# Optimization experiments

Hardware: AMD Instinct MI355X
Metric: run time of the kernel (lower is better)

Reference implementation:

```python
import jax, jax.numpy as jnp
import numpy as np

N = 30000        # nodes
E_EDGES = 960000 # edges (avg degree 32)
G = 16           # graphs in batch
D_IN, D_H, D_OUT = 6, 256, 256
L = 3            # GraphConv layers per expert
N_EXP, TOP_K = 8, 2


def _lin(key, fan_in, shape):
    return jax.random.normal(key, shape, dtype=jnp.float32) / np.sqrt(fan_in)


def setup_inputs() -> dict:
    key = jax.random.key(0)
    ks = jax.random.split(key, 12)
    x = jax.random.normal(ks[0], (N, D_IN), dtype=jnp.float32)
    edge_index = jax.random.randint(ks[1], (2, E_EDGES), 0, N, dtype=jnp.int64)
    batch = jnp.sort(jax.random.randint(ks[2], (N,), 0, G, dtype=jnp.int64))
    return {
        "x": x,
        "edge_index": edge_index,
        "batch": batch,
        # SharedBusEncoder: Linear(in, hidden) + ReLU
        "enc_W": _lin(ks[3], D_IN, (D_IN, D_H)),
        "enc_b": jnp.zeros((D_H,), jnp.float32),
        # BaseRouter: Linear(hidden+2, hidden) -> ReLU -> Linear(hidden, n_experts)
        "r_W1": _lin(ks[4], D_H + 2, (D_H + 2, D_H)),
        "r_b1": jnp.zeros((D_H,), jnp.float32),
        "r_W2": _lin(ks[5], D_H, (D_H, N_EXP)),
        "r_b2": jnp.zeros((N_EXP,), jnp.float32),
        # GraphConvExpert: L layers of PyG GraphConv (lin_rel on aggregated
        # neighbors + lin_root on self), stacked over [layer, expert].
        "Wrel": _lin(ks[6], D_H, (L, N_EXP, D_H, D_OUT)),
        "brel": jnp.zeros((L, N_EXP, D_OUT), jnp.float32),
        "Wroot": _lin(ks[7], D_H, (L, N_EXP, D_H, D_OUT)),
    }


def _forward(x, edge_index, batch, enc_W, enc_b, r_W1, r_b1, r_W2, r_b2,
             Wrel, brel, Wroot):
    src, dst = edge_index[0], edge_index[1]
    # encoder
    h = jax.nn.relu(x @ enc_W + enc_b)  # [N, D_H]

    # graph size features: per-node [log(#nodes), log(#edges)] of its graph
    n_g = jax.ops.segment_sum(jnp.ones((N,), jnp.float32), batch, num_segments=G)
    e_g = jax.ops.segment_sum(jnp.ones((E_EDGES,), jnp.float32), batch[src], num_segments=G)
    size = jnp.log(jnp.maximum(jnp.stack([n_g, e_g], axis=-1), 1.0))  # [G, 2]
    size_feat = size[batch]  # [N, 2]

    # router + sparse top-k routing
    r_h = jax.nn.relu(jnp.concatenate([h, size_feat], axis=-1) @ r_W1 + r_b1)
    logits = r_h @ r_W2 + r_b2            # [N, E]
    probs = jax.nn.softmax(logits, axis=-1)
    vals, idx = jax.lax.top_k(probs, TOP_K)
    vals = vals / jnp.sum(vals, axis=-1, keepdims=True)
    sparse = jnp.zeros((N, N_EXP), probs.dtype).at[
        jnp.arange(N)[:, None], idx].set(vals)  # [N, E]

    # all-expert GraphConv stacks (dense over experts, as in the original)
    agg0 = jax.ops.segment_sum(h[src], dst, num_segments=N)  # [N, D_H]
    H = jnp.einsum('nd,edf->enf', agg0, Wrel[0]) + brel[0][:, None, :] \
        + jnp.einsum('nd,edf->enf', h, Wroot[0])             # [E, N, D]
    for l in range(1, L):
        H = jax.nn.relu(H)
        A = jax.vmap(lambda hh: jax.ops.segment_sum(hh[src], dst, num_segments=N))(H)
        H = jnp.einsum('end,edf->enf', A, Wrel[l]) + brel[l][:, None, :] \
            + jnp.einsum('end,edf->enf', H, Wroot[l])

    # mask-and-sum combine
    return jnp.einsum('enf,ne->nf', H, sparse)  # [N, D_OUT]


def reference(x, edge_index, batch, enc_W, enc_b, r_W1, r_b1, r_W2, r_b2,
              Wrel, brel, Wroot):
    return _forward(x, edge_index, batch, enc_W, enc_b, r_W1, r_b1, r_W2,
                    r_b2, Wrel, brel, Wroot)
```

## Files before the change

kernel.cpp:

```cpp
#include <hip/hip_runtime.h>
#include <hip/hip_bf16.h>
#include <math.h>

#define NEXP 8
#define GNUM 16
#define DH 256

typedef __attribute__((ext_vector_type(8))) short s16x8;
typedef __attribute__((ext_vector_type(4))) float f32x4;
typedef unsigned short u16;
typedef unsigned int u32;

__device__ __forceinline__ float bitsToF(u32 b){ union{u32 u; float f;} c; c.u=b; return c.f; }
__device__ __forceinline__ u16 f2bf(float f){
  union{float f; u32 u;} c; c.f=f;
  u32 r = c.u + 0x7fffu + ((c.u>>16)&1u);
  return (u16)(r>>16);
}

#define GLOAD_LDS16(gp, lp) __builtin_amdgcn_global_load_lds( \
    (const __attribute__((address_space(1))) unsigned int*)(gp), \
    (__attribute__((address_space(3))) unsigned int*)(lp), 16, 0, 0)

__global__ void count_edges_k(const int* __restrict__ ei, const int* __restrict__ batch,
                              int* __restrict__ deg, int* __restrict__ eg, int E){
  __shared__ int leg[GNUM];
  int t = threadIdx.x;
  if (t < GNUM) leg[t] = 0;
  __syncthreads();
  int i = blockIdx.x*blockDim.x + t;
  if (i < E){
    int s = ei[i];
    int d = ei[E + i];
    atomicAdd(&deg[d], 1);
    atomicAdd(&leg[batch[s]], 1);
  }
  __syncthreads();
  if (t < GNUM){ int v = leg[t]; if (v) atomicAdd(&eg[t], v); }
}

__global__ void count_nodes_k(const int* __restrict__ batch, int* __restrict__ ng, int N){
  __shared__ int lng[GNUM];
  int t = threadIdx.x;
  if (t < GNUM) lng[t] = 0;
  __syncthreads();
  int i = blockIdx.x*blockDim.x + t;
  if (i < N) atomicAdd(&lng[batch[i]], 1);
  __syncthreads();
  if (t < GNUM){ int v = lng[t]; if (v) atomicAdd(&ng[t], v); }
}

#define SCAN_T 1024
#define SCAN_CH 32
__global__ __launch_bounds__(1024) void scan_deg_k(const int* __restrict__ deg,
    int* __restrict__ row_ptr, int* __restrict__ cursor, int N){
  __shared__ int part[SCAN_T];
  int t = threadIdx.x;
  int base = t*SCAN_CH;
  int loc[SCAN_CH];
  int s = 0;
  #pragma unroll
  for (int j=0;j<SCAN_CH;j++){
    int i = base+j;
    int v = (i<N)? deg[i] : 0;
    loc[j] = s; s += v;
  }
  part[t] = s;
  __syncthreads();
  for (int off=1; off<SCAN_T; off<<=1){
    int add = (t>=off)? part[t-off] : 0;
    __syncthreads();
    part[t] += add;
    __syncthreads();
  }
  int ex = (t==0)? 0 : part[t-1];
  #pragma unroll
  for (int j=0;j<SCAN_CH;j++){
    int i = base+j;
    if (i<N){ int v = ex + loc[j]; row_ptr[i]=v; cursor[i]=v; }
  }
  if (t == SCAN_T-1) row_ptr[N] = part[SCAN_T-1];
}

__global__ void scatter_edges_k(const int* __restrict__ ei, int* __restrict__ cursor,
                                int* __restrict__ csr_src, int E){
  int i = blockIdx.x*blockDim.x + threadIdx.x;
  if (i>=E) return;
  int s = ei[i];
  int d = ei[E + i];
  int pos = atomicAdd(&cursor[d], 1);
  csr_src[pos] = s;
}

__global__ void size_feats_k(const int* __restrict__ ng, const int* __restrict__ eg,
                             float* __restrict__ sizef){
  int g = threadIdx.x;
  if (g < GNUM){
    sizef[g*2]   = logf(fmaxf((float)ng[g], 1.f));
    sizef[g*2+1] = logf(fmaxf((float)eg[g], 1.f));
  }
}

__global__ void mark_fail_k(float* out){ out[0] = __builtin_nanf(""); }

__global__ __launch_bounds__(256) void encoder_k(const float* __restrict__ x,
    const float* __restrict__ W, const float* __restrict__ b,
    float* __restrict__ hf, u16* __restrict__ bh, int N){
  int n = blockIdx.x; if (n>=N) return;
  int f = threadIdx.x;
  float acc = b[f];
  #pragma unroll
  for (int k=0;k<6;k++) acc += x[n*6+k]*W[k*DH+f];
  acc = fmaxf(acc, 0.f);
  hf[(size_t)n*DH+f] = acc;
  bh[(size_t)n*DH+f] = f2bf(acc);
}

__global__ __launch_bounds__(256) void convw_k(const float* __restrict__ Wrel,
    const float* __restrict__ Wroot, u16* __restrict__ WT){
  __shared__ float tile[64][65];
  int tx = threadIdx.x;
  int ty = threadIdx.y;
  int kt = blockIdx.x & 3, ct = blockIdx.x >> 2;
  int srcRoot = blockIdx.y;
  int le = blockIdx.z;
  const float* src = (srcRoot ? Wroot : Wrel) + (size_t)le*65536;
  #pragma unroll
  for (int i=0;i<16;i++){
    int kl = ty + i*4;
    tile[kl][tx] = src[(size_t)(kt*64 + kl)*256 + ct*64 + tx];
  }
  __syncthreads();
  u16* dst = WT + (size_t)le*131072 + (srcRoot ? 256 : 0) + kt*64;
  #pragma unroll
  for (int i=0;i<16;i++){
    int cl = ty + i*4;
    dst[(size_t)(ct*64 + cl)*512 + tx] = f2bf(tile[tx][cl]);
  }
}

#define R1N 32
__global__ __launch_bounds__(256) void router1_k(
    const float* __restrict__ hf, const float* __restrict__ sizef,
    const int* __restrict__ batch,
    const float* __restrict__ W1, const float* __restrict__ b1,
    float* __restrict__ rh, int N)
{
  __shared__ float xin[R1N][264];
  int t = threadIdx.x;
  int lane = t & 63, w = t >> 6;
  int n0 = blockIdx.x * R1N;
  #pragma unroll
  for (int i=0;i<R1N;i++){
    int n = n0 + i;
    xin[i][t] = (n<N) ? hf[(size_t)n*DH + t] : 0.f;
  }
  if (t < R1N){
    int n = n0 + t;
    int g = (n<N) ? (int)batch[n] : 0;
    xin[t][256] = sizef[g*2];
    xin[t][257] = sizef[g*2+1];
    xin[t][258] = 0.f; xin[t][259] = 0.f;
    xin[t][260] = 0.f; xin[t][261] = 0.f; xin[t][262] = 0.f; xin[t][263] = 0.f;
  }
  __syncthreads();

  int wn = w*8;
  float bb[4];
  #pragma unroll
  for (int c=0;c<4;c++) bb[c] = b1[lane + c*64];
  float acc[8][4];
  #pragma unroll
  for (int i=0;i<8;i++)
    #pragma unroll
    for (int c=0;c<4;c++) acc[i][c] = bb[c];

  #pragma unroll 2
  for (int k4=0; k4<256; k4+=4){
    float w4[4][4];
    #pragma unroll
    for (int j=0;j<4;j++)
      #pragma unroll
      for (int c=0;c<4;c++)
        w4[j][c] = W1[(size_t)(k4+j)*DH + lane + c*64];
    #pragma unroll
    for (int i=0;i<8;i++){
      f32x4 xv = *(const f32x4*)&xin[wn+i][k4];
      #pragma unroll
      for (int j=0;j<4;j++)
        #pragma unroll
        for (int c=0;c<4;c++)
          acc[i][c] += xv[j]*w4[j][c];
    }
  }
  float w256[4], w257[4];
  #pragma unroll
  for (int c=0;c<4;c++){
    w256[c] = W1[(size_t)256*DH + lane + c*64];
    w257[c] = W1[(size_t)257*DH + lane + c*64];
  }
  #pragma unroll
  for (int i=0;i<8;i++){
    float s0 = xin[wn+i][256], s1 = xin[wn+i][257];
    #pragma unroll
    for (int c=0;c<4;c++) acc[i][c] += s0*w256[c] + s1*w257[c];
  }
  #pragma unroll
  for (int i=0;i<8;i++){
    int n = n0 + wn + i;
    if (n < N){
      #pragma unroll
      for (int c=0;c<4;c++)
        rh[(size_t)n*DH + lane + c*64] = fmaxf(acc[i][c], 0.f);
    }
  }
}

__global__ __launch_bounds__(256) void router2_k(
    const float* __restrict__ rh, const float* __restrict__ W2,
    const float* __restrict__ b2,
    int* __restrict__ ridx, float* __restrict__ rval, int N)
{
  __shared__ float w2s[NEXP][260];
  int t = threadIdx.x;
  for (int i=t; i<NEXP*DH; i+=256){
    int e = i >> 8, k = i & 255;
    w2s[e][k] = W2[(size_t)k*NEXP + e];
  }
  __syncthreads();
  int lane = t & 63, w = t >> 6;
  int n = blockIdx.x*4 + w;
  if (n >= N) return;
  const float* r = rh + (size_t)n*DH;
  float p[NEXP];
  #pragma unroll
  for (int e=0;e<NEXP;e++) p[e] = 0.f;
  #pragma unroll
  for (int c=0;c<4;c++){
    int k = lane + c*64;
    float rv = r[k];
    #pragma unroll
    for (int e=0;e<NEXP;e++) p[e] += rv * w2s[e][k];
  }
  #pragma unroll
  for (int off=1; off<64; off<<=1){
    #pragma unroll
    for (int e=0;e<NEXP;e++) p[e] += __shfl_xor(p[e], off, 64);
  }
  if (lane == 0){
    float l0[NEXP];
    #pragma unroll
    for (int e=0;e<NEXP;e++) l0[e] = p[e] + b2[e];
    float m = l0[0];
    #pragma unroll
    for (int e=1;e<NEXP;e++) m = fmaxf(m, l0[e]);
    float ex[NEXP];
    #pragma unroll
    for (int e=0;e<NEXP;e++) ex[e] = expf(l0[e]-m);
    int e0=0; float b0v=ex[0];
    #pragma unroll
    for (int e=1;e<NEXP;e++) if (ex[e]>b0v){b0v=ex[e]; e0=e;}
    int e1=(e0==0)?1:0; float b1v=ex[e1];
    #pragma unroll
    for (int e=0;e<NEXP;e++) if (e!=e0 && ex[e]>b1v){b1v=ex[e]; e1=e;}
    float sv = b0v + b1v;
    rval[n*2]   = b0v/sv;
    rval[n*2+1] = b1v/sv;
    ridx[n*2]   = e0;
    ridx[n*2+1] = e1;
  }
}

__global__ __launch_bounds__(256) void rsort_k(const int* __restrict__ ridx,
    int* __restrict__ cnt, int* __restrict__ plist, int* __restrict__ ppos, int N){
  __shared__ int lcnt[NEXP];
  __shared__ int lbase[NEXP];
  int t = threadIdx.x;
  int n = blockIdx.x*256 + t;
  if (t < NEXP) lcnt[t] = 0;
  __syncthreads();
  int e0=0, e1=0, o0=0, o1=0;
  if (n < N){
    e0 = ridx[n*2];
    e1 = ridx[n*2+1];
    o0 = atomicAdd(&lcnt[e0], 1);
    o1 = atomicAdd(&lcnt[e1], 1);
  }
  __syncthreads();
  if (t < NEXP) lbase[t] = atomicAdd(&cnt[t], lcnt[t]);
  __syncthreads();
  if (n < N){
    int p0 = lbase[e0] + o0;
    int p1 = lbase[e1] + o1;
    plist[(size_t)e0*N + p0] = n;
    plist[(size_t)e1*N + p1] = n;
    ppos[n*2]   = p0;
    ppos[n*2+1] = p1;
  }
}

__device__ __forceinline__ void agg_row(const u16* __restrict__ H,
    u16* __restrict__ Arow, const int* __restrict__ row_ptr,
    const int* __restrict__ csr_src, int node, int lane){
  int beg = row_ptr[node], end = row_ptr[node+1];
  float a0=0.f,a1=0.f,a2=0.f,a3=0.f;
  const u16* Hl = H + (lane<<2);
  int i = beg;
  for (; i+8<=end; i+=8){
    int sarr[8];
    #pragma unroll
    for (int u=0;u<8;u++) sarr[u] = csr_src[i+u];
    #pragma unroll
    for (int u=0;u<8;u++){
      uint2 v = *(const uint2*)(Hl + ((size_t)sarr[u]<<8));
      a0 += bitsToF(v.x<<16);
      a1 += bitsToF(v.x & 0xffff0000u);
      a2 += bitsToF(v.y<<16);
      a3 += bitsToF(v.y & 0xffff0000u);
    }
  }
  for (; i<end; ++i){
    int s = csr_src[i];
    uint2 v = *(const uint2*)(Hl + ((size_t)s<<8));
    a0 += bitsToF(v.x<<16);
    a1 += bitsToF(v.x & 0xffff0000u);
    a2 += bitsToF(v.y<<16);
    a3 += bitsToF(v.y & 0xffff0000u);
  }
  uint2 o;
  o.x = ((u32)f2bf(a1)<<16) | f2bf(a0);
  o.y = ((u32)f2bf(a3)<<16) | f2bf(a2);
  *(uint2*)(Arow + (lane<<2)) = o;
}

__global__ __launch_bounds__(256) void agg0_k(const u16* __restrict__ H,
    u16* __restrict__ A, const int* __restrict__ row_ptr,
    const int* __restrict__ csr_src, int N){
  int node = blockIdx.x*4 + (threadIdx.x>>6);
  if (node >= N) return;
  int lane = threadIdx.x & 63;
  agg_row(H, A + ((size_t)node<<8), row_ptr, csr_src, node, lane);
}

__global__ __launch_bounds__(256) void agg1g_k(const u16* __restrict__ Hsrc,
    u16* __restrict__ Aout, const int* __restrict__ row_ptr,
    const int* __restrict__ csr_src, int N, int ezMask, int ezShift){
  int bid = blockIdx.x;
  int el = bid & ezMask;
  int xb = bid >> ezShift;
  int node = xb*4 + (threadIdx.x>>6);
  if (node >= N) return;
  int lane = threadIdx.x & 63;
  size_t NS = (size_t)N*DH;
  agg_row(Hsrc + (size_t)el*NS, Aout + (size_t)el*NS + ((size_t)node<<8),
          row_ptr, csr_src, node, lane);
}

__global__ __launch_bounds__(256) void agg2sg_k(const u16* __restrict__ Hsrc,
    u16* __restrict__ Aout, u16* __restrict__ Rout,
    const int* __restrict__ row_ptr, const int* __restrict__ csr_src,
    const int* __restrict__ plist, const int* __restrict__ cnt,
    int N, int gBase){
  int el = blockIdx.y;
  int idx = blockIdx.x*4 + (threadIdx.x>>6);
  if (idx >= cnt[gBase + el]) return;
  int node = plist[(size_t)(gBase + el)*N + idx];
  size_t NS = (size_t)N*DH;
  const u16* H = Hsrc + (size_t)el*NS;
  int lane = threadIdx.x & 63;
  uint2 rootv = *(const uint2*)(H + ((size_t)node<<8) + (lane<<2));
  agg_row(H, Aout + (size_t)el*NS + ((size_t)idx<<8), row_ptr, csr_src, node, lane);
  *(uint2*)(Rout + (size_t)el*NS + ((size_t)idx<<8) + (lane<<2)) = rootv;
}

__device__ __forceinline__ void gemm_dense_body(
    const u16* __restrict__ aBase, const u16* __restrict__ rBase,
    const u16* __restrict__ wBase, const float* __restrict__ be,
    u16* __restrict__ Oe, int N, int relu_flag, u16* As, u16* Bs)
{
  int tid = threadIdx.x;
  int lane = tid & 63, w = tid >> 6;
  int wr = w >> 1, wc = w & 1;
  int m0 = blockIdx.x * 128;
  int n0 = blockIdx.y * 128;

  int lrow = lane >> 2;
  int q8   = (((lane & 3) ^ ((lane >> 3) & 3))) * 8;
  int r0 = w*16 + lrow;
  int r1 = (w+4)*16 + lrow;
  int arow0 = m0 + r0; if (arow0 >= N) arow0 = N-1;
  int arow1 = m0 + r1; if (arow1 >= N) arow1 = N-1;
  long long aoff0 = (long long)arow0*256 + q8;
  long long aoff1 = (long long)arow1*256 + q8;
  long long boff0 = (long long)(n0 + r0)*512 + q8;
  long long boff1 = (long long)(n0 + r1)*512 + q8;
  u16* aL0 = As + (size_t)w*512;
  u16* aL1 = As + (size_t)(w+4)*512;
  u16* bL0 = Bs + (size_t)w*512;
  u16* bL1 = Bs + (size_t)(w+4)*512;

  f32x4 acc[4][4];
  #pragma unroll
  for (int a=0;a<4;a++)
    #pragma unroll
    for (int b=0;b<4;b++) acc[a][b] = (f32x4){0.f,0.f,0.f,0.f};

  int fr = lane & 15;
  int fk = (((lane >> 4) ^ ((fr >> 1) & 3))) * 8;
  const u16* aRead = As + (size_t)(wr*64 + fr)*32 + fk;
  const u16* bRead = Bs + (size_t)(wc*64 + fr)*32 + fk;

  #pragma unroll 1
  for (int half=0; half<2; ++half){
    const u16* sA = half ? rBase : aBase;
    #pragma unroll 1
    for (int kk=0; kk<8; ++kk){
      int kin = kk*32;
      int kg  = half*256 + kin;
      GLOAD_LDS16(sA + aoff0 + kin, aL0);
      GLOAD_LDS16(sA + aoff1 + kin, aL1);
      GLOAD_LDS16(wBase + boff0 + kg, bL0);
      GLOAD_LDS16(wBase + boff1 + kg, bL1);
      __syncthreads();
      s16x8 af[4], bf[4];
      #pragma unroll
      for (int mi=0;mi<4;mi++) af[mi] = *(const s16x8*)(aRead + mi*16*32);
      #pragma unroll
      for (int ni=0;ni<4;ni++) bf[ni] = *(const s16x8*)(bRead + ni*16*32);
      #pragma unroll
      for (int mi=0;mi<4;mi++)
        #pragma unroll
        for (int ni=0;ni<4;ni++)
          acc[mi][ni] = __builtin_amdgcn_mfma_f32_16x16x32_bf16(af[mi], bf[ni], acc[mi][ni], 0, 0, 0);
      __syncthreads();
    }
  }
  int fq = lane >> 4;
  #pragma unroll
  for (int ni=0;ni<4;ni++){
    int col = n0 + wc*64 + ni*16 + fr;
    float bv = be[col];
    #pragma unroll
    for (int mi=0;mi<4;mi++){
      int rowb = m0 + wr*64 + mi*16 + fq*4;
      f32x4 v = acc[mi][ni];
      #pragma unroll
      for (int j=0;j<4;j++){
        int row = rowb + j;
        if (row < N){
          float o = v[j] + bv;
          if (relu_flag) o = fmaxf(o, 0.f);
          Oe[(size_t)row*DH + col] = f2bf(o);
        }
      }
    }
  }
}

__global__ __launch_bounds__(256,2) void gemm0g_k(
    const u16* __restrict__ A0, const u16* __restrict__ bh,
    const u16* __restrict__ WT, const float* __restrict__ bias,
    u16* __restrict__ Hout, int N){
  __shared__ u16 As[128*32];
  __shared__ u16 Bs[128*32];
  int el = blockIdx.z;
  gemm_dense_body(A0, bh, WT + (size_t)el*(256*512), bias + el*256,
                  Hout + (size_t)el*((size_t)N*DH), N, 1, As, Bs);
}
__global__ __launch_bounds__(256,2) void gemm1g_k(
    const u16* __restrict__ Aagg, const u16* __restrict__ Hroot,
    const u16* __restrict__ WT, const float* __restrict__ bias,
    u16* __restrict__ Hout, int N){
  __shared__ u16 As[128*32];
  __shared__ u16 Bs[128*32];
  int el = blockIdx.z;
  size_t NS = (size_t)N*DH;
  gemm_dense_body(Aagg + (size_t)el*NS, Hroot + (size_t)el*NS,
                  WT + (size_t)el*(256*512), bias + el*256,
                  Hout + (size_t)el*NS, N, 1, As, Bs);
}

__global__ __launch_bounds__(256,2) void gemm2sg_k(
    const u16* __restrict__ Aagg, const u16* __restrict__ Rc,
    const u16* __restrict__ WT, const float* __restrict__ bias,
    u16* __restrict__ Hout, const int* __restrict__ cnte, int N, int gBase)
{
  __shared__ u16 As[128*32];
  __shared__ u16 Bs[128*32];
  int el = blockIdx.z;
  int cnt = cnte[gBase + el];
  int m0 = blockIdx.x * 128;
  if (m0 >= cnt) return;
  size_t NS = (size_t)N*DH;
  const u16* aBase = Aagg + (size_t)el*NS;
  const u16* rBase = Rc + (size_t)el*NS;
  const u16* wBase = WT + (size_t)el*(256*512);
  const float* be  = bias + el*256;
  u16* Oe = Hout + (size_t)el*NS;

  int tid = threadIdx.x;
  int lane = tid & 63, w = tid >> 6;
  int wr = w >> 1, wc = w & 1;
  int n0 = blockIdx.y * 128;

  int lrow = lane >> 2;
  int q8   = (((lane & 3) ^ ((lane >> 3) & 3))) * 8;
  int r0 = w*16 + lrow;
  int r1 = (w+4)*16 + lrow;
  int ai0 = m0 + r0; if (ai0 >= cnt) ai0 = cnt-1;
  int ai1 = m0 + r1; if (ai1 >= cnt) ai1 = cnt-1;
  long long aoff0 = (long long)ai0*256 + q8;
  long long aoff1 = (long long)ai1*256 + q8;
  long long boff0 = (long long)(n0 + r0)*512 + q8;
  long long boff1 = (long long)(n0 + r1)*512 + q8;
  u16* aL0 = As + (size_t)w*512;
  u16* aL1 = As + (size_t)(w+4)*512;
  u16* bL0 = Bs + (size_t)w*512;
  u16* bL1 = Bs + (size_t)(w+4)*512;

  f32x4 acc[4][4];
  #pragma unroll
  for (int a=0;a<4;a++)
    #pragma unroll
    for (int b=0;b<4;b++) acc[a][b] = (f32x4){0.f,0.f,0.f,0.f};

  int fr = lane & 15;
  int fk = (((lane >> 4) ^ ((fr >> 1) & 3))) * 8;
  const u16* aRead = As + (size_t)(wr*64 + fr)*32 + fk;
  const u16* bRead = Bs + (size_t)(wc*64 + fr)*32 + fk;

  #pragma unroll 1
  for (int half=0; half<2; ++half){
    const u16* sA = half ? rBase : aBase;
    #pragma unroll 1
    for (int kk=0; kk<8; ++kk){
      int kin = kk*32;
      int kg  = half*256 + kin;
      GLOAD_LDS16(sA + aoff0 + kin, aL0);
      GLOAD_LDS16(sA + aoff1 + kin, aL1);
      GLOAD_LDS16(wBase + boff0 + kg, bL0);
      GLOAD_LDS16(wBase + boff1 + kg, bL1);
      __syncthreads();
      s16x8 af[4], bf[4];
      #pragma unroll
      for (int mi=0;mi<4;mi++) af[mi] = *(const s16x8*)(aRead + mi*16*32);
      #pragma unroll
      for (int ni=0;ni<4;ni++) bf[ni] = *(const s16x8*)(bRead + ni*16*32);
      #pragma unroll
      for (int mi=0;mi<4;mi++)
        #pragma unroll
        for (int ni=0;ni<4;ni++)
          acc[mi][ni] = __builtin_amdgcn_mfma_f32_16x16x32_bf16(af[mi], bf[ni], acc[mi][ni], 0, 0, 0);
      __syncthreads();
    }
  }
  int fq = lane >> 4;
  #pragma unroll
  for (int ni=0;ni<4;ni++){
    int col = n0 + wc*64 + ni*16 + fr;
    float bv = be[col];
    #pragma unroll
    for (int mi=0;mi<4;mi++){
      int rowb = m0 + wr*64 + mi*16 + fq*4;
      f32x4 v = acc[mi][ni];
      #pragma unroll
      for (int j=0;j<4;j++){
        int row = rowb + j;
        if (row < cnt){
          float o = v[j] + bv;
          Oe[(size_t)row*DH + col] = f2bf(o);
        }
      }
    }
  }
}

__global__ __launch_bounds__(256) void combine_spg_k(const u16* __restrict__ H3c,
    const int* __restrict__ ridx, const int* __restrict__ ppos,
    const float* __restrict__ rval, float* __restrict__ out,
    int N, int gBase, int ezCnt, int first){
  int n = blockIdx.x; if (n>=N) return;
  int f = threadIdx.x;
  size_t NS = (size_t)N*DH;
  size_t off = (size_t)n*DH + f;
  float acc = first ? 0.f : out[off];
  #pragma unroll
  for (int p=0;p<2;p++){
    int el = ridx[n*2+p] - gBase;
    if (el >= 0 && el < ezCnt)
      acc += rval[n*2+p] * bitsToF(((u32)H3c[(size_t)el*NS + (size_t)ppos[n*2+p]*DH + f])<<16);
  }
  out[off] = acc;
}

extern "C" void kernel_launch(void* const* d_in, const int* in_sizes, int n_in,
                              void* d_out, int out_size, void* d_ws, size_t ws_size,
                              hipStream_t stream)
{
  const float* x    = (const float*)d_in[0];
  const int*   ei   = (const int*)d_in[1];
  const int*   batch= (const int*)d_in[2];
  const float* encW = (const float*)d_in[3];
  const float* encb = (const float*)d_in[4];
  const float* rW1  = (const float*)d_in[5];
  const float* rb1  = (const float*)d_in[6];
  const float* rW2  = (const float*)d_in[7];
  const float* rb2  = (const float*)d_in[8];
  const float* Wrel = (const float*)d_in[9];
  const float* brel = (const float*)d_in[10];
  const float* Wroot= (const float*)d_in[11];
  int N = in_sizes[2];
  int E = in_sizes[1]/2;
  float* out = (float*)d_out;
  (void)n_in; (void)out_size;

  size_t NS = (size_t)N*DH;
  char* p = (char*)d_ws;
  auto carve = [&](size_t bytes)->char*{
    char* r = p; p += (bytes + 255) & ~(size_t)255; return r;
  };
  u16*  bh   = (u16*)carve(NS*2);
  u16*  WT   = (u16*)carve((size_t)3*NEXP*256*512*2);
  int*  deg  = (int*)carve((size_t)N*4 + 64*4);
  int*  ng   = deg + N;
  int*  eg   = ng + GNUM;
  int*  row_ptr = (int*)carve(((size_t)N+1)*4);
  int*  cursor  = (int*)carve((size_t)N*4);
  int*  csr     = (int*)carve((size_t)E*4);
  float* sizef  = (float*)carve(GNUM*2*4);
  int*  ridx    = (int*)carve((size_t)N*2*4);
  float* rvalv  = (float*)carve((size_t)N*2*4);
  int*  ecnt    = (int*)carve(NEXP*4);
  int*  plist   = (int*)carve((size_t)NEXP*N*4);
  int*  ppos    = (int*)carve((size_t)N*2*4);
  u16*  A0      = (u16*)carve(NS*2);
  size_t baseUsed = (size_t)(p - (char*)d_ws);

  int EZ = 0;
  for (int cand = NEXP; cand >= 1; cand >>= 1){
    if (baseUsed + (size_t)cand*3*NS*2 <= ws_size){ EZ = cand; break; }
  }
  if (EZ == 0){ mark_fail_k<<<1,1,0,stream>>>(out); return; }
  int ezShift = (EZ==8)?3 : (EZ==4)?2 : (EZ==2)?1 : 0;

  u16* Abuf = (u16*)carve((size_t)EZ*NS*2);
  u16* Hc   = (u16*)carve((size_t)EZ*NS*2);
  u16* Hn   = (u16*)carve((size_t)EZ*NS*2);
  float* hf; float* rh;
  if (EZ >= 2){ hf = (float*)Abuf; rh = (float*)Hn; }
  else {
    hf = (float*)carve(NS*4);
    rh = (float*)carve(NS*4);
    if ((size_t)(p - (char*)d_ws) > ws_size){ mark_fail_k<<<1,1,0,stream>>>(out); return; }
  }

  hipMemsetAsync(deg, 0, (size_t)N*4 + (size_t)2*GNUM*4, stream);
  hipMemsetAsync(ecnt, 0, NEXP*4, stream);

  int eb = (E + 255)/256;
  count_edges_k<<<eb, 256, 0, stream>>>(ei, batch, deg, eg, E);
  count_nodes_k<<<(N+255)/256, 256, 0, stream>>>(batch, ng, N);
  scan_deg_k<<<1, SCAN_T, 0, stream>>>(deg, row_ptr, cursor, N);
  scatter_edges_k<<<eb, 256, 0, stream>>>(ei, cursor, csr, E);
  size_feats_k<<<1, 64, 0, stream>>>(ng, eg, sizef);
  encoder_k<<<N, 256, 0, stream>>>(x, encW, encb, hf, bh, N);
  convw_k<<<dim3(16,2,3*NEXP), dim3(64,4), 0, stream>>>(Wrel, Wroot, WT);
  router1_k<<<(N+R1N-1)/R1N, 256, 0, stream>>>(hf, sizef, batch, rW1, rb1, rh, N);
  router2_k<<<(N+3)/4, 256, 0, stream>>>(rh, rW2, rb2, ridx, rvalv, N);
  rsort_k<<<(N+255)/256, 256, 0, stream>>>(ridx, ecnt, plist, ppos, N);

  int aggx = (N+3)/4;
  int mt = (N+127)/128;
  const size_t WE = (size_t)256*512;

  agg0_k<<<aggx, 256, 0, stream>>>(bh, A0, row_ptr, csr, N);

  for (int g = 0; g < NEXP; g += EZ){
    gemm0g_k<<<dim3(mt,2,EZ), 256, 0, stream>>>(A0, bh,
        WT + ((size_t)0*NEXP + g)*WE, brel + (0*NEXP + g)*256, Hc, N);
    agg1g_k<<<aggx*EZ, 256, 0, stream>>>(Hc, Abuf, row_ptr, csr, N, EZ-1, ezShift);
    gemm1g_k<<<dim3(mt,2,EZ), 256, 0, stream>>>(Abuf, Hc,
        WT + ((size_t)1*NEXP + g)*WE, brel + (1*NEXP + g)*256, Hn, N);
    agg2sg_k<<<dim3(aggx,EZ), 256, 0, stream>>>(Hn, Abuf, Hc, row_ptr, csr,
        plist, ecnt, N, g);
    gemm2sg_k<<<dim3(mt,2,EZ), 256, 0, stream>>>(Abuf, Hc,
        WT + ((size_t)2*NEXP + g)*WE, brel + (2*NEXP + g)*256, Hn, ecnt, N, g);
    combine_spg_k<<<N, 256, 0, stream>>>(Hn, ridx, ppos, rvalv, out, N, g, EZ, g==0);
  }
}
```

Measured before the change: 1.303 ms.

## Fuse neighbor aggregation into layer-1 and layer-2 expert GEMMs via LDS A-tile

```diff
diff --git a/kernel.cpp b/kernel.cpp
--- a/kernel.cpp
+++ b/kernel.cpp
@@ -21,6 +21,17 @@
 #define GLOAD_LDS16(gp, lp) __builtin_amdgcn_global_load_lds( \
     (const __attribute__((address_space(1))) unsigned int*)(gp), \
     (__attribute__((address_space(3))) unsigned int*)(lp), 16, 0, 0)
+
+__device__ __forceinline__ u16* as_swz(u16* As, int r, int e){
+  unsigned byte = ((unsigned)r << 10) + ((unsigned)e << 1);
+  byte ^= ((unsigned)(r & 7)) << 4;
+  return (u16*)((char*)As + byte);
+}
+__device__ __forceinline__ const u16* as_swz_c(const u16* As, int r, int e){
+  unsigned byte = ((unsigned)r << 10) + ((unsigned)e << 1);
+  byte ^= ((unsigned)(r & 7)) << 4;
+  return (const u16*)((const char*)As + byte);
+}
 
 __global__ void count_edges_k(const int* __restrict__ ei, const int* __restrict__ batch,
                               int* __restrict__ deg, int* __restrict__ eg, int E){
@@ -342,42 +353,178 @@
   agg_row(H, A + ((size_t)node<<8), row_ptr, csr_src, node, lane);
 }
 
-__global__ __launch_bounds__(256) void agg1g_k(const u16* __restrict__ Hsrc,
-    u16* __restrict__ Aout, const int* __restrict__ row_ptr,
-    const int* __restrict__ csr_src, int N, int ezMask, int ezShift){
-  int bid = blockIdx.x;
-  int el = bid & ezMask;
-  int xb = bid >> ezShift;
-  int node = xb*4 + (threadIdx.x>>6);
-  if (node >= N) return;
-  int lane = threadIdx.x & 63;
+template<int SPARSE>
+__device__ __forceinline__ void fgemm_body(
+    const u16* __restrict__ H,
+    const u16* __restrict__ wBase,
+    const float* __restrict__ be,
+    u16* __restrict__ Oe,
+    const int* __restrict__ row_ptr, const int* __restrict__ csr_src,
+    const int* __restrict__ rows,
+    int cnt, int relu_flag,
+    u16* As, u16* Bs)
+{
+  int tid = threadIdx.x;
+  int lane = tid & 63, w = tid >> 6;
+  int m0 = blockIdx.x * 64;
+
+  #pragma unroll 1
+  for (int i=0;i<16;i++){
+    int r = w*16 + i;
+    int grow = m0 + r;
+    if (grow < cnt){
+      int node = SPARSE ? rows[grow] : grow;
+      uint2 rv = *(const uint2*)(H + ((size_t)node<<8) + (lane<<2));
+      *(uint2*)as_swz(As, r, 256 + (lane<<2)) = rv;
+      int beg = row_ptr[node], end = row_ptr[node+1];
+      float a0=0.f,a1=0.f,a2=0.f,a3=0.f;
+      const u16* Hl = H + (lane<<2);
+      int ii = beg;
+      for (; ii+8<=end; ii+=8){
+        int sarr[8];
+        #pragma unroll
+        for (int u=0;u<8;u++) sarr[u] = csr_src[ii+u];
+        #pragma unroll
+        for (int u=0;u<8;u++){
+          uint2 v = *(const uint2*)(Hl + ((size_t)sarr[u]<<8));
+          a0 += bitsToF(v.x<<16);
+          a1 += bitsToF(v.x & 0xffff0000u);
+          a2 += bitsToF(v.y<<16);
+          a3 += bitsToF(v.y & 0xffff0000u);
+        }
+      }
+      for (; ii<end; ++ii){
+        int s = csr_src[ii];
+        uint2 v = *(const uint2*)(Hl + ((size_t)s<<8));
+        a0 += bitsToF(v.x<<16);
+        a1 += bitsToF(v.x & 0xffff0000u);
+        a2 += bitsToF(v.y<<16);
+        a3 += bitsToF(v.y & 0xffff0000u);
+      }
+      uint2 o;
+      o.x = ((u32)f2bf(a1)<<16) | f2bf(a0);
+      o.y = ((u32)f2bf(a3)<<16) | f2bf(a2);
+      *(uint2*)as_swz(As, r, (lane<<2)) = o;
+    } else {
+      uint2 z; z.x = 0u; z.y = 0u;
+      *(uint2*)as_swz(As, r, (lane<<2)) = z;
+      *(uint2*)as_swz(As, r, 256 + (lane<<2)) = z;
+    }
+  }
+  __syncthreads();
+
+  int wr = w >> 1, wc = w & 1;
+  int fr = lane & 15;
+  int fkA = (lane >> 4) * 8;
+  int q8  = (((lane & 3) ^ ((lane >> 3) & 3))) * 8;
+  int fkB = (((lane >> 4) ^ ((fr >> 1) & 3))) * 8;
+
+  long long boffs[4];
+  u16* bL[4];
+  #pragma unroll
+  for (int j=0;j<4;j++){
+    int c = w + 4*j;
+    int col = c*16 + (lane >> 2);
+    boffs[j] = (long long)col*512 + q8;
+    bL[j] = Bs + (size_t)c*512;
+  }
+
+  f32x4 acc[2][8];
+  #pragma unroll
+  for (int a=0;a<2;a++)
+    #pragma unroll
+    for (int b=0;b<8;b++) acc[a][b] = (f32x4){0.f,0.f,0.f,0.f};
+
+  int rowA0 = wr*32 + fr;
+  int rowA1 = wr*32 + 16 + fr;
+  const u16* bRead = Bs + (size_t)(wc*128 + fr)*32 + fkB;
+
+  #pragma unroll 1
+  for (int kk=0; kk<16; ++kk){
+    int k0e = kk*32;
+    #pragma unroll
+    for (int j=0;j<4;j++) GLOAD_LDS16(wBase + boffs[j] + k0e, bL[j]);
+    __syncthreads();
+    s16x8 af[2], bf[8];
+    af[0] = *(const s16x8*)as_swz_c(As, rowA0, fkA + k0e);
+    af[1] = *(const s16x8*)as_swz_c(As, rowA1, fkA + k0e);
+    #pragma unroll
+    for (int ni=0;ni<8;ni++) bf[ni] = *(const s16x8*)(bRead + (size_t)ni*16*32);
+    #pragma unroll
+    for (int mi=0;mi<2;mi++)
+      #pragma unroll
+      for (int ni=0;ni<8;ni++)
+        acc[mi][ni] = __builtin_amdgcn_mfma_f32_16x16x32_bf16(af[mi], bf[ni], acc[mi][ni], 0, 0, 0);
+    __syncthreads();
+  }
+
+  int fq = lane >> 4;
+  #pragma unroll
+  for (int ni=0;ni<8;ni++){
+    int col = wc*128 + ni*16 + fr;
+    float bv = be[col];
+    #pragma unroll
+    for (int mi=0;mi<2;mi++){
+      int rowb = m0 + wr*32 + mi*16 + fq*4;
+      f32x4 v = acc[mi][ni];
+      #pragma unroll
+      for (int j=0;j<4;j++){
+        int row = rowb + j;
+        if (row < cnt){
+          float o = v[j] + bv;
+          if (relu_flag) o = fmaxf(o, 0.f);
+          Oe[(size_t)row*DH + col] = f2bf(o);
+        }
+      }
+    }
+  }
+}
+
+__global__ __launch_bounds__(256,2) void fgemm1_k(
+    const u16* __restrict__ Hsrc, const u16* __restrict__ WT,
+    const float* __restrict__ bias, u16* __restrict__ Hout,
+    const int* __restrict__ row_ptr, const int* __restrict__ csr_src, int N)
+{
+  __shared__ u16 As[64*512];
+  __shared__ u16 Bs[256*32];
+  int el = blockIdx.z;
   size_t NS = (size_t)N*DH;
-  agg_row(Hsrc + (size_t)el*NS, Aout + (size_t)el*NS + ((size_t)node<<8),
-          row_ptr, csr_src, node, lane);
-}
-
-__global__ __launch_bounds__(256) void agg2sg_k(const u16* __restrict__ Hsrc,
-    u16* __restrict__ Aout, u16* __restrict__ Rout,
+  fgemm_body<0>(Hsrc + (size_t)el*NS, WT + (size_t)el*(256*512), bias + el*256,
+                Hout + (size_t)el*NS, row_ptr, csr_src, nullptr, N, 1, As, Bs);
+}
+
+__global__ __launch_bounds__(256,2) void fgemm2s_k(
+    const u16* __restrict__ Hsrc, const u16* __restrict__ WT,
+    const float* __restrict__ bias, u16* __restrict__ Hout,
     const int* __restrict__ row_ptr, const int* __restrict__ csr_src,
-    const int* __restrict__ plist, const int* __restrict__ cnt,
-    int N, int gBase){
-  int el = blockIdx.y;
-  int idx = blockIdx.x*4 + (threadIdx.x>>6);
-  if (idx >= cnt[gBase + el]) return;
-  int node = plist[(size_t)(gBase + el)*N + idx];
+    const int* __restrict__ plist, const int* __restrict__ cnte,
+    int N, int gBase)
+{
+  __shared__ u16 As[64*512];
+  __shared__ u16 Bs[256*32];
+  int el = blockIdx.z;
+  int cnt = cnte[gBase + el];
+  if ((int)(blockIdx.x*64) >= cnt) return;
   size_t NS = (size_t)N*DH;
-  const u16* H = Hsrc + (size_t)el*NS;
-  int lane = threadIdx.x & 63;
-  uint2 rootv = *(const uint2*)(H + ((size_t)node<<8) + (lane<<2));
-  agg_row(H, Aout + (size_t)el*NS + ((size_t)idx<<8), row_ptr, csr_src, node, lane);
-  *(uint2*)(Rout + (size_t)el*NS + ((size_t)idx<<8) + (lane<<2)) = rootv;
-}
-
-__device__ __forceinline__ void gemm_dense_body(
-    const u16* __restrict__ aBase, const u16* __restrict__ rBase,
-    const u16* __restrict__ wBase, const float* __restrict__ be,
-    u16* __restrict__ Oe, int N, int relu_flag, u16* As, u16* Bs)
+  fgemm_body<1>(Hsrc + (size_t)el*NS, WT + (size_t)el*(256*512), bias + el*256,
+                Hout + (size_t)el*NS, row_ptr, csr_src,
+                plist + (size_t)(gBase + el)*N, cnt, 0, As, Bs);
+}
+
+__global__ __launch_bounds__(256,2) void gemm0g_k(
+    const u16* __restrict__ A0, const u16* __restrict__ bh,
+    const u16* __restrict__ WT, const float* __restrict__ bias,
+    u16* __restrict__ Hout, int N)
 {
+  __shared__ u16 As[128*32];
+  __shared__ u16 Bs[128*32];
+  int el = blockIdx.z;
+  const u16* aBase = A0;
+  const u16* rBase = bh;
+  const u16* wBase = WT + (size_t)el*(256*512);
+  const float* be  = bias + el*256;
+  u16* Oe = Hout + (size_t)el*((size_t)N*DH);
+
   int tid = threadIdx.x;
   int lane = tid & 63, w = tid >> 6;
   int wr = w >> 1, wc = w & 1;
@@ -449,125 +596,7 @@
         int row = rowb + j;
         if (row < N){
           float o = v[j] + bv;
-          if (relu_flag) o = fmaxf(o, 0.f);
-          Oe[(size_t)row*DH + col] = f2bf(o);
-        }
-      }
-    }
-  }
-}
-
-__global__ __launch_bounds__(256,2) void gemm0g_k(
-    const u16* __restrict__ A0, const u16* __restrict__ bh,
-    const u16* __restrict__ WT, const float* __restrict__ bias,
-    u16* __restrict__ Hout, int N){
-  __shared__ u16 As[128*32];
-  __shared__ u16 Bs[128*32];
-  int el = blockIdx.z;
-  gemm_dense_body(A0, bh, WT + (size_t)el*(256*512), bias + el*256,
-                  Hout + (size_t)el*((size_t)N*DH), N, 1, As, Bs);
-}
-__global__ __launch_bounds__(256,2) void gemm1g_k(
-    const u16* __restrict__ Aagg, const u16* __restrict__ Hroot,
-    const u16* __restrict__ WT, const float* __restrict__ bias,
-    u16* __restrict__ Hout, int N){
-  __shared__ u16 As[128*32];
-  __shared__ u16 Bs[128*32];
-  int el = blockIdx.z;
-  size_t NS = (size_t)N*DH;
-  gemm_dense_body(Aagg + (size_t)el*NS, Hroot + (size_t)el*NS,
-                  WT + (size_t)el*(256*512), bias + el*256,
-                  Hout + (size_t)el*NS, N, 1, As, Bs);
-}
-
-__global__ __launch_bounds__(256,2) void gemm2sg_k(
-    const u16* __restrict__ Aagg, const u16* __restrict__ Rc,
-    const u16* __restrict__ WT, const float* __restrict__ bias,
-    u16* __restrict__ Hout, const int* __restrict__ cnte, int N, int gBase)
-{
-  __shared__ u16 As[128*32];
-  __shared__ u16 Bs[128*32];
-  int el = blockIdx.z;
-  int cnt = cnte[gBase + el];
-  int m0 = blockIdx.x * 128;
-  if (m0 >= cnt) return;
-  size_t NS = (size_t)N*DH;
-  const u16* aBase = Aagg + (size_t)el*NS;
-  const u16* rBase = Rc + (size_t)el*NS;
-  const u16* wBase = WT + (size_t)el*(256*512);
-  const float* be  = bias + el*256;
-  u16* Oe = Hout + (size_t)el*NS;
-
-  int tid = threadIdx.x;
-  int lane = tid & 63, w = tid >> 6;
-  int wr = w >> 1, wc = w & 1;
-  int n0 = blockIdx.y * 128;
-
-  int lrow = lane >> 2;
-  int q8   = (((lane & 3) ^ ((lane >> 3) & 3))) * 8;
-  int r0 = w*16 + lrow;
-  int r1 = (w+4)*16 + lrow;
-  int ai0 = m0 + r0; if (ai0 >= cnt) ai0 = cnt-1;
-  int ai1 = m0 + r1; if (ai1 >= cnt) ai1 = cnt-1;
-  long long aoff0 = (long long)ai0*256 + q8;
-  long long aoff1 = (long long)ai1*256 + q8;
-  long long boff0 = (long long)(n0 + r0)*512 + q8;
-  long long boff1 = (long long)(n0 + r1)*512 + q8;
-  u16* aL0 = As + (size_t)w*512;
-  u16* aL1 = As + (size_t)(w+4)*512;
-  u16* bL0 = Bs + (size_t)w*512;
-  u16* bL1 = Bs + (size_t)(w+4)*512;
-
-  f32x4 acc[4][4];
-  #pragma unroll
-  for (int a=0;a<4;a++)
-    #pragma unroll
-    for (int b=0;b<4;b++) acc[a][b] = (f32x4){0.f,0.f,0.f,0.f};
-
-  int fr = lane & 15;
-  int fk = (((lane >> 4) ^ ((fr >> 1) & 3))) * 8;
-  const u16* aRead = As + (size_t)(wr*64 + fr)*32 + fk;
-  const u16* bRead = Bs + (size_t)(wc*64 + fr)*32 + fk;
-
-  #pragma unroll 1
-  for (int half=0; half<2; ++half){
-    const u16* sA = half ? rBase : aBase;
-    #pragma unroll 1
-    for (int kk=0; kk<8; ++kk){
-      int kin = kk*32;
-      int kg  = half*256 + kin;
-      GLOAD_LDS16(sA + aoff0 + kin, aL0);
-      GLOAD_LDS16(sA + aoff1 + kin, aL1);
-      GLOAD_LDS16(wBase + boff0 + kg, bL0);
-      GLOAD_LDS16(wBase + boff1 + kg, bL1);
-      __syncthreads();
-      s16x8 af[4], bf[4];
-      #pragma unroll
-      for (int mi=0;mi<4;mi++) af[mi] = *(const s16x8*)(aRead + mi*16*32);
-      #pragma unroll
-      for (int ni=0;ni<4;ni++) bf[ni] = *(const s16x8*)(bRead + ni*16*32);
-      #pragma unroll
-      for (int mi=0;mi<4;mi++)
-        #pragma unroll
-        for (int ni=0;ni<4;ni++)
-          acc[mi][ni] = __builtin_amdgcn_mfma_f32_16x16x32_bf16(af[mi], bf[ni], acc[mi][ni], 0, 0, 0);
-      __syncthreads();
-    }
-  }
-  int fq = lane >> 4;
-  #pragma unroll
-  for (int ni=0;ni<4;ni++){
-    int col = n0 + wc*64 + ni*16 + fr;
-    float bv = be[col];
-    #pragma unroll
-    for (int mi=0;mi<4;mi++){
-      int rowb = m0 + wr*64 + mi*16 + fq*4;
-      f32x4 v = acc[mi][ni];
-      #pragma unroll
-      for (int j=0;j<4;j++){
-        int row = rowb + j;
-        if (row < cnt){
-          float o = v[j] + bv;
+          o = fmaxf(o, 0.f);
           Oe[(size_t)row*DH + col] = f2bf(o);
         }
       }
@@ -638,16 +667,14 @@
 
   int EZ = 0;
   for (int cand = NEXP; cand >= 1; cand >>= 1){
-    if (baseUsed + (size_t)cand*3*NS*2 <= ws_size){ EZ = cand; break; }
+    if (baseUsed + (size_t)cand*2*NS*2 <= ws_size){ EZ = cand; break; }
   }
   if (EZ == 0){ mark_fail_k<<<1,1,0,stream>>>(out); return; }
-  int ezShift = (EZ==8)?3 : (EZ==4)?2 : (EZ==2)?1 : 0;
-
-  u16* Abuf = (u16*)carve((size_t)EZ*NS*2);
-  u16* Hc   = (u16*)carve((size_t)EZ*NS*2);
-  u16* Hn   = (u16*)carve((size_t)EZ*NS*2);
+
+  u16* Hc = (u16*)carve((size_t)EZ*NS*2);
+  u16* Hn = (u16*)carve((size_t)EZ*NS*2);
   float* hf; float* rh;
-  if (EZ >= 2){ hf = (float*)Abuf; rh = (float*)Hn; }
+  if (EZ >= 2){ hf = (float*)Hc; rh = (float*)Hn; }
   else {
     hf = (float*)carve(NS*4);
     rh = (float*)carve(NS*4);
@@ -670,21 +697,21 @@
   rsort_k<<<(N+255)/256, 256, 0, stream>>>(ridx, ecnt, plist, ppos, N);
 
   int aggx = (N+3)/4;
-  int mt = (N+127)/128;
+  int mt128 = (N+127)/128;
+  int mt64  = (N+63)/64;
   const size_t WE = (size_t)256*512;
 
   agg0_k<<<aggx, 256, 0, stream>>>(bh, A0, row_ptr, csr, N);
 
   for (int g = 0; g < NEXP; g += EZ){
-    gemm0g_k<<<dim3(mt,2,EZ), 256, 0, stream>>>(A0, bh,
+    gemm0g_k<<<dim3(mt128,2,EZ), 256, 0, stream>>>(A0, bh,
         WT + ((size_t)0*NEXP + g)*WE, brel + (0*NEXP + g)*256, Hc, N);
-    agg1g_k<<<aggx*EZ, 256, 0, stream>>>(Hc, Abuf, row_ptr, csr, N, EZ-1, ezShift);
-    gemm1g_k<<<dim3(mt,2,EZ), 256, 0, stream>>>(Abuf, Hc,
-        WT + ((size_t)1*NEXP + g)*WE, brel + (1*NEXP + g)*256, Hn, N);
-    agg2sg_k<<<dim3(aggx,EZ), 256, 0, stream>>>(Hn, Abuf, Hc, row_ptr, csr,
-        plist, ecnt, N, g);
-    gemm2sg_k<<<dim3(mt,2,EZ), 256, 0, stream>>>(Abuf, Hc,
-        WT + ((size_t)2*NEXP + g)*WE, brel + (2*NEXP + g)*256, Hn, ecnt, N, g);
-    combine_spg_k<<<N, 256, 0, stream>>>(Hn, ridx, ppos, rvalv, out, N, g, EZ, g==0);
-  }
-}
+    fgemm1_k<<<dim3(mt64,1,EZ), 256, 0, stream>>>(Hc,
+        WT + ((size_t)1*NEXP + g)*WE, brel + (1*NEXP + g)*256, Hn,
+        row_ptr, csr, N);
+    fgemm2s_k<<<dim3(mt64,1,EZ), 256, 0, stream>>>(Hn,
+        WT + ((size_t)2*NEXP + g)*WE, brel + (2*NEXP + g)*256, Hc,
+        row_ptr, csr, plist, ecnt, N, g);
+    combine_spg_k<<<N, 256, 0, stream>>>(Hc, ridx, ppos, rvalv, out, N, g, EZ, g==0);
+  }
+}
```

After: 1.743 ms. 1.34x slower.

## Use BK=64 K-tiles with XOR-swizzled LDS in dense expert GEMMs; split layer-1 aggregation

Applied to the files above, without the earlier changes.

```diff
diff --git a/kernel.cpp b/kernel.cpp
--- a/kernel.cpp
+++ b/kernel.cpp
@@ -342,18 +342,31 @@
   agg_row(H, A + ((size_t)node<<8), row_ptr, csr_src, node, lane);
 }
 
-__global__ __launch_bounds__(256) void agg1g_k(const u16* __restrict__ Hsrc,
+__device__ __forceinline__ void agg1_body(const u16* __restrict__ Hsrc,
     u16* __restrict__ Aout, const int* __restrict__ row_ptr,
-    const int* __restrict__ csr_src, int N, int ezMask, int ezShift){
+    const int* __restrict__ csr_src, int N, int base, int cntN,
+    int ezMask, int ezShift){
   int bid = blockIdx.x;
   int el = bid & ezMask;
   int xb = bid >> ezShift;
-  int node = xb*4 + (threadIdx.x>>6);
-  if (node >= N) return;
+  int node = base + xb*4 + (threadIdx.x>>6);
+  if (node >= base + cntN) return;
   int lane = threadIdx.x & 63;
   size_t NS = (size_t)N*DH;
   agg_row(Hsrc + (size_t)el*NS, Aout + (size_t)el*NS + ((size_t)node<<8),
           row_ptr, csr_src, node, lane);
+}
+__global__ __launch_bounds__(256) void agg1a_k(const u16* __restrict__ Hsrc,
+    u16* __restrict__ Aout, const int* __restrict__ row_ptr,
+    const int* __restrict__ csr_src, int N, int base, int cntN,
+    int ezMask, int ezShift){
+  agg1_body(Hsrc, Aout, row_ptr, csr_src, N, base, cntN, ezMask, ezShift);
+}
+__global__ __launch_bounds__(256) void agg1b_k(const u16* __restrict__ Hsrc,
+    u16* __restrict__ Aout, const int* __restrict__ row_ptr,
+    const int* __restrict__ csr_src, int N, int base, int cntN,
+    int ezMask, int ezShift){
+  agg1_body(Hsrc, Aout, row_ptr, csr_src, N, base, cntN, ezMask, ezShift);
 }
 
 __global__ __launch_bounds__(256) void agg2sg_k(const u16* __restrict__ Hsrc,
@@ -373,7 +386,7 @@
   *(uint2*)(Rout + (size_t)el*NS + ((size_t)idx<<8) + (lane<<2)) = rootv;
 }
 
-__device__ __forceinline__ void gemm_dense_body(
+__device__ __forceinline__ void gemm_bk64_body(
     const u16* __restrict__ aBase, const u16* __restrict__ rBase,
     const u16* __restrict__ wBase, const float* __restrict__ be,
     u16* __restrict__ Oe, int N, int relu_flag, u16* As, u16* Bs)
@@ -384,20 +397,20 @@
   int m0 = blockIdx.x * 128;
   int n0 = blockIdx.y * 128;
 
-  int lrow = lane >> 2;
-  int q8   = (((lane & 3) ^ ((lane >> 3) & 3))) * 8;
-  int r0 = w*16 + lrow;
-  int r1 = (w+4)*16 + lrow;
-  int arow0 = m0 + r0; if (arow0 >= N) arow0 = N-1;
-  int arow1 = m0 + r1; if (arow1 >= N) arow1 = N-1;
-  long long aoff0 = (long long)arow0*256 + q8;
-  long long aoff1 = (long long)arow1*256 + q8;
-  long long boff0 = (long long)(n0 + r0)*512 + q8;
-  long long boff1 = (long long)(n0 + r1)*512 + q8;
-  u16* aL0 = As + (size_t)w*512;
-  u16* aL1 = As + (size_t)(w+4)*512;
-  u16* bL0 = Bs + (size_t)w*512;
-  u16* bL1 = Bs + (size_t)(w+4)*512;
+  int lr8 = lane >> 3;
+  int p   = (lane & 7) ^ lr8;
+  long long asrc[4]; u16* aL[4];
+  long long bsrc[4]; u16* bL[4];
+  #pragma unroll
+  for (int j=0;j<4;j++){
+    int c = w*4 + j;
+    int arow = m0 + c*8 + lr8; if (arow >= N) arow = N-1;
+    asrc[j] = (long long)arow*256 + p*8;
+    aL[j] = As + (size_t)c*512;
+    int bcol = n0 + c*8 + lr8;
+    bsrc[j] = (long long)bcol*512 + p*8;
+    bL[j] = Bs + (size_t)c*512;
+  }
 
   f32x4 acc[4][4];
   #pragma unroll
@@ -406,35 +419,43 @@
     for (int b=0;b<4;b++) acc[a][b] = (f32x4){0.f,0.f,0.f,0.f};
 
   int fr = lane & 15;
-  int fk = (((lane >> 4) ^ ((fr >> 1) & 3))) * 8;
-  const u16* aRead = As + (size_t)(wr*64 + fr)*32 + fk;
-  const u16* bRead = Bs + (size_t)(wc*64 + fr)*32 + fk;
+  int fkq = lane >> 4;
 
   #pragma unroll 1
-  for (int half=0; half<2; ++half){
-    const u16* sA = half ? rBase : aBase;
-    #pragma unroll 1
-    for (int kk=0; kk<8; ++kk){
-      int kin = kk*32;
-      int kg  = half*256 + kin;
-      GLOAD_LDS16(sA + aoff0 + kin, aL0);
-      GLOAD_LDS16(sA + aoff1 + kin, aL1);
-      GLOAD_LDS16(wBase + boff0 + kg, bL0);
-      GLOAD_LDS16(wBase + boff1 + kg, bL1);
-      __syncthreads();
+  for (int kk=0; kk<8; ++kk){
+    const u16* sA = (kk < 4) ? aBase : rBase;
+    int koff = (kk & 3) * 64;
+    #pragma unroll
+    for (int j=0;j<4;j++){
+      GLOAD_LDS16(sA + asrc[j] + koff, aL[j]);
+      GLOAD_LDS16(wBase + bsrc[j] + kk*64, bL[j]);
+    }
+    __syncthreads();
+    #pragma unroll
+    for (int kin=0; kin<2; ++kin){
+      unsigned fb = (unsigned)(fkq*16 + kin*64);
       s16x8 af[4], bf[4];
       #pragma unroll
-      for (int mi=0;mi<4;mi++) af[mi] = *(const s16x8*)(aRead + mi*16*32);
-      #pragma unroll
-      for (int ni=0;ni<4;ni++) bf[ni] = *(const s16x8*)(bRead + ni*16*32);
+      for (int mi=0;mi<4;mi++){
+        int row = wr*64 + mi*16 + fr;
+        unsigned byte = ((unsigned)row << 7) + (fb ^ (((unsigned)(row & 7)) << 4));
+        af[mi] = *(const s16x8*)((const char*)As + byte);
+      }
+      #pragma unroll
+      for (int ni=0;ni<4;ni++){
+        int col = wc*64 + ni*16 + fr;
+        unsigned byte = ((unsigned)col << 7) + (fb ^ (((unsigned)(col & 7)) << 4));
+        bf[ni] = *(const s16x8*)((const char*)Bs + byte);
+      }
       #pragma unroll
       for (int mi=0;mi<4;mi++)
         #pragma unroll
         for (int ni=0;ni<4;ni++)
           acc[mi][ni] = __builtin_amdgcn_mfma_f32_16x16x32_bf16(af[mi], bf[ni], acc[mi][ni], 0, 0, 0);
-      __syncthreads();
     }
-  }
+    __syncthreads();
+  }
+
   int fq = lane >> 4;
   #pragma unroll
   for (int ni=0;ni<4;ni++){
@@ -461,23 +482,23 @@
     const u16* __restrict__ A0, const u16* __restrict__ bh,
     const u16* __restrict__ WT, const float* __restrict__ bias,
     u16* __restrict__ Hout, int N){
-  __shared__ u16 As[128*32];
-  __shared__ u16 Bs[128*32];
+  __shared__ u16 As[128*64];
+  __shared__ u16 Bs[128*64];
   int el = blockIdx.z;
-  gemm_dense_body(A0, bh, WT + (size_t)el*(256*512), bias + el*256,
-                  Hout + (size_t)el*((size_t)N*DH), N, 1, As, Bs);
+  gemm_bk64_body(A0, bh, WT + (size_t)el*(256*512), bias + el*256,
+                 Hout + (size_t)el*((size_t)N*DH), N, 1, As, Bs);
 }
 __global__ __launch_bounds__(256,2) void gemm1g_k(
     const u16* __restrict__ Aagg, const u16* __restrict__ Hroot,
     const u16* __restrict__ WT, const float* __restrict__ bias,
     u16* __restrict__ Hout, int N){
-  __shared__ u16 As[128*32];
-  __shared__ u16 Bs[128*32];
+  __shared__ u16 As[128*64];
+  __shared__ u16 Bs[128*64];
   int el = blockIdx.z;
   size_t NS = (size_t)N*DH;
-  gemm_dense_body(Aagg + (size_t)el*NS, Hroot + (size_t)el*NS,
-                  WT + (size_t)el*(256*512), bias + el*256,
-                  Hout + (size_t)el*NS, N, 1, As, Bs);
+  gemm_bk64_body(Aagg + (size_t)el*NS, Hroot + (size_t)el*NS,
+                 WT + (size_t)el*(256*512), bias + el*256,
+                 Hout + (size_t)el*NS, N, 1, As, Bs);
 }
 
 __global__ __launch_bounds__(256,2) void gemm2sg_k(
@@ -670,20 +691,28 @@
   rsort_k<<<(N+255)/256, 256, 0, stream>>>(ridx, ecnt, plist, ppos, N);
 
   int aggx = (N+3)/4;
-  int mt = (N+127)/128;
+  int mt128 = (N+127)/128;
   const size_t WE = (size_t)256*512;
 
   agg0_k<<<aggx, 256, 0, stream>>>(bh, A0, row_ptr, csr, N);
 
+  int half0 = (((N+1)/2) + 3) & ~3;
+  if (half0 > N) half0 = N;
+  int half1 = N - half0;
+  int g1a = ((half0+3)/4)*EZ;
+  int g1b = ((half1+3)/4)*EZ;
+
   for (int g = 0; g < NEXP; g += EZ){
-    gemm0g_k<<<dim3(mt,2,EZ), 256, 0, stream>>>(A0, bh,
+    gemm0g_k<<<dim3(mt128,2,EZ), 256, 0, stream>>>(A0, bh,
         WT + ((size_t)0*NEXP + g)*WE, brel + (0*NEXP + g)*256, Hc, N);
-    agg1g_k<<<aggx*EZ, 256, 0, stream>>>(Hc, Abuf, row_ptr, csr, N, EZ-1, ezShift);
-    gemm1g_k<<<dim3(mt,2,EZ), 256, 0, stream>>>(Abuf, Hc,
+    agg1a_k<<<g1a, 256, 0, stream>>>(Hc, Abuf, row_ptr, csr, N, 0, half0, EZ-1, ezShift);
+    if (half1 > 0)
+      agg1b_k<<<g1b, 256, 0, stream>>>(Hc, Abuf, row_ptr, csr, N, half0, half1, EZ-1, ezShift);
+    gemm1g_k<<<dim3(mt128,2,EZ), 256, 0, stream>>>(Abuf, Hc,
         WT + ((size_t)1*NEXP + g)*WE, brel + (1*NEXP + g)*256, Hn, N);
     agg2sg_k<<<dim3(aggx,EZ), 256, 0, stream>>>(Hn, Abuf, Hc, row_ptr, csr,
         plist, ecnt, N, g);
-    gemm2sg_k<<<dim3(mt,2,EZ), 256, 0, stream>>>(Abuf, Hc,
+    gemm2sg_k<<<dim3(mt128,2,EZ), 256, 0, stream>>>(Abuf, Hc,
         WT + ((size_t)2*NEXP + g)*WE, brel + (2*NEXP + g)*256, Hn, ecnt, N, g);
     combine_spg_k<<<N, 256, 0, stream>>>(Hn, ridx, ppos, rvalv, out, N, g, EZ, g==0);
   }
```

After: 1.295 ms, median of 2. About the same (-0.6%).
